# Kernel tuning notes

Measured on AMD Instinct MI355X. Metric: run time of the kernel, lower is better.

## Reference

```python
import jax, jax.numpy as jnp
import numpy as np

OUT = 128
HEADS = 8
HEAD = OUT // HEADS
NEG_SLOPE = 0.01


def _seg_softmax(logits, seg, num_segments):
    # logits: [E, H]; seg: [E] receiver node ids
    mx = jax.ops.segment_max(logits, seg, num_segments=num_segments)
    e = jnp.exp(logits - mx[seg])
    s = jax.ops.segment_sum(e, seg, num_segments=num_segments)
    return e / s[seg]


def _gat_pass(z, src, tgt, extra_logits, Wm, bm, Wa1, ba1, Wa2, ba2):
    # z: [N, 2D]; src/tgt: [E]; extra_logits: [E, H] or None
    N = z.shape[0]
    att1 = z @ Wa1 + ba1  # [N, H]
    att2 = z @ Wa2 + ba2  # [N, H]
    logits = att1[src] + att2[tgt]
    if extra_logits is not None:
        logits = logits + extra_logits
    coefs = _seg_softmax(jax.nn.leaky_relu(logits, NEG_SLOPE), tgt, N)  # [E, H]
    v = (z @ Wm + bm).reshape(N, HEADS, HEAD)  # [N, H, hs]
    msg = coefs[..., None] * v[src]            # [E, H, hs]
    agg = jax.ops.segment_sum(msg, tgt, num_segments=N)  # [N, H, hs]
    return agg.reshape(N, OUT)


def setup_inputs() -> dict:
    key = jax.random.key(0)
    ks = jax.random.split(key, 16)
    B, N, D, E = 2, 32768, 128, 262144
    ZD = 2 * D  # concat(node_fts, hidden)
    inp = {
        "node_fts": jax.random.normal(ks[0], (B, N, D), jnp.float32),
        "gkt_edge_fts": jax.random.normal(ks[1], (B, E, D), jnp.float32),
        "hidden": jax.random.normal(ks[2], (B, N, D), jnp.float32),
        "cfg_indices_padded": jax.random.randint(ks[3], (B, E, 2), 0, N, jnp.int32),
        "gkt_indices_padded": jax.random.randint(ks[4], (B, E, 2), 0, N, jnp.int32),
        "Wm": jax.random.normal(ks[5], (ZD, OUT), jnp.float32) / np.sqrt(ZD),
        "bm": jnp.zeros((OUT,), jnp.float32),
        "Wskip": jax.random.normal(ks[6], (ZD, OUT), jnp.float32) / np.sqrt(ZD),
        "bskip": jnp.zeros((OUT,), jnp.float32),
        "Wa1": jax.random.normal(ks[7], (ZD, HEADS), jnp.float32) / np.sqrt(ZD),
        "ba1": jnp.zeros((HEADS,), jnp.float32),
        "Wa2": jax.random.normal(ks[8], (ZD, HEADS), jnp.float32) / np.sqrt(ZD),
        "ba2": jnp.zeros((HEADS,), jnp.float32),
        "Wae": jax.random.normal(ks[9], (D, HEADS), jnp.float32) / np.sqrt(D),
        "bae": jnp.zeros((HEADS,), jnp.float32),
    }
    return inp


def reference(node_fts, gkt_edge_fts, hidden, cfg_indices_padded, gkt_indices_padded,
              Wm, bm, Wskip, bskip, Wa1, ba1, Wa2, ba2, Wae, bae):
    cfg_src = cfg_indices_padded[..., 0]
    cfg_tgt = cfg_indices_padded[..., 1]
    gkt_src = gkt_indices_padded[..., 0]
    gkt_tgt = gkt_indices_padded[..., 1]

    # ---- cfg stage ----
    cfg_z = jnp.concatenate([node_fts, hidden], axis=-1)  # [B, N, 2D]

    def cfg_one(z_b, src_b, tgt_b):
        return _gat_pass(z_b, src_b, tgt_b, None, Wm, bm, Wa1, ba1, Wa2, ba2)

    cfg_hidden = jax.vmap(cfg_one)(cfg_z, cfg_src, cfg_tgt)  # [B, N, OUT]
    cfg_hidden = cfg_hidden + cfg_z @ Wskip + bskip  # residual skip
    cfg_hidden = jax.nn.relu(cfg_hidden)

    # ---- gkt stage ----
    gkt_z = jnp.concatenate([node_fts, cfg_hidden], axis=-1)  # [B, N, 2D]
    gkt_att_e = gkt_edge_fts @ Wae + bae  # [B, E, H]

    def gkt_one(z_b, src_b, tgt_b, ae_b):
        return _gat_pass(z_b, src_b, tgt_b, ae_b, Wm, bm, Wa1, ba1, Wa2, ba2)

    ret = jax.vmap(gkt_one)(gkt_z, gkt_src, gkt_tgt, gkt_att_e)  # [B, N, OUT]
    ret = ret + gkt_z @ Wskip + bskip
    ret = jax.nn.relu(ret)
    return ret
```

## Files before the change

kernel.cpp:

```cpp
#include <hip/hip_runtime.h>
#include <hip/hip_bf16.h>

#define NB 2
#define NN 32768
#define NE 262144
#define DD 128
#define ZD 256
#define HEADS 8
#define OUTD 128
#define CAP 64

typedef short s16x8 __attribute__((ext_vector_type(8)));
typedef float f32x4 __attribute__((ext_vector_type(4)));
#define MFMA(a,b,c) __builtin_amdgcn_mfma_f32_16x16x32_bf16((a),(b),(c),0,0,0)

__device__ inline ushort f2bf(float f) {
    union { float f; unsigned u; } c; c.f = f;
    unsigned u = c.u;
    unsigned r = (u + 0x7fffu + ((u >> 16) & 1u)) >> 16;
    return (ushort)r;
}
__device__ inline float bf2f(ushort u) {
    union { unsigned u; float f; } c; c.u = ((unsigned)u) << 16;
    return c.f;
}

__global__ __launch_bounds__(256) void pack_w(
    const float* __restrict__ Wm, const float* __restrict__ Wsk,
    const float* __restrict__ Wa1, const float* __restrict__ Wa2,
    const float* __restrict__ bm, const float* __restrict__ bsk,
    const float* __restrict__ ba1, const float* __restrict__ ba2,
    ushort* __restrict__ WT, float* __restrict__ bias)
{
    int c = blockIdx.x;
    int k = threadIdx.x;
    float val;
    if (c < 32) {
        int a = c & 15;
        float w = (a < 8) ? Wa1[k*8 + a] : Wa2[k*8 + (a - 8)];
        if (c < 16) val = w;
        else { ushort hi = f2bf(w); val = w - bf2f(hi); }
    } else if (c < 160) {
        val = Wm[k*128 + (c - 32)];
    } else {
        val = Wsk[k*128 + (c - 160)];
    }
    WT[((size_t)(k >> 5)*288 + c)*32 + (k & 31)] = f2bf(val);
    if (k == 0) {
        if (c < 16) bias[c] = (c < 8) ? ba1[c] : ba2[c - 8];
        else if (c >= 32) bias[c - 16] = (c < 160) ? bm[c - 32] : bsk[c - 160];
    }
}

__global__ __launch_bounds__(256) void bucket_kernel(
    const int* __restrict__ cfg, const int* __restrict__ gkt,
    int* __restrict__ cnt, int2* __restrict__ pairs)
{
    int gid = blockIdx.x*256 + threadIdx.x;
    int L = gid >> 18, e = gid & (NE - 1);
    const int* base = (L < 2) ? cfg : gkt;
    const int* ip = base + (((size_t)(L & 1) << 18) + e)*2;
    int src = ip[0], tgt = ip[1];
    int pos = atomicAdd(&cnt[(L << 15) + tgt], 1);
    if (pos < CAP)
        pairs[((size_t)((L << 15) + tgt) << 6) + pos] = make_int2(e, src);
}

__global__ __launch_bounds__(256) void edge_att(
    const float* __restrict__ efts, const float* __restrict__ Wae,
    const float* __restrict__ bae, float* __restrict__ out)
{
    int t = threadIdx.x, lane = t & 63, wid = t >> 6;
    int col = lane & 15, q = lane >> 4;
    s16x8 bf[4];
    #pragma unroll
    for (int kc = 0; kc < 4; ++kc) {
        #pragma unroll
        for (int j = 0; j < 8; ++j) {
            float wv = (col < 8) ? Wae[(kc*32 + q*8 + j)*8 + col] : 0.f;
            bf[kc][j] = (short)f2bf(wv);
        }
    }
    float bb = (col < 8) ? bae[col] : 0.f;
    int wg = blockIdx.x*4 + wid;
    const int NT = (NB*NE)/16;
    for (int tile = wg; tile < NT; tile += gridDim.x*4) {
        size_t row = (size_t)tile*16 + col;
        const float* rp = efts + row*128 + q*8;
        f32x4 acc = {0.f, 0.f, 0.f, 0.f};
        #pragma unroll
        for (int kc = 0; kc < 4; ++kc) {
            float4 x0 = *(const float4*)(rp + kc*32);
            float4 x1 = *(const float4*)(rp + kc*32 + 4);
            s16x8 af;
            af[0] = (short)f2bf(x0.x); af[1] = (short)f2bf(x0.y);
            af[2] = (short)f2bf(x0.z); af[3] = (short)f2bf(x0.w);
            af[4] = (short)f2bf(x1.x); af[5] = (short)f2bf(x1.y);
            af[6] = (short)f2bf(x1.z); af[7] = (short)f2bf(x1.w);
            acc = MFMA(af, bf[kc], acc);
        }
        if (col < 8) {
            size_t e0 = (size_t)tile*16 + q*4;
            #pragma unroll
            for (int r = 0; r < 4; ++r)
                out[(e0 + r)*8 + col] = acc[r] + bb;
        }
    }
}

__global__ __launch_bounds__(256) void gemm_nodes(
    const float* __restrict__ nf, const float* __restrict__ h2,
    const ushort* __restrict__ WT, const float* __restrict__ bias,
    float* __restrict__ att1, float* __restrict__ att2,
    float* __restrict__ vout, float* __restrict__ skip)
{
    constexpr int LDA = 264;
    __shared__ ushort Ah[32*LDA];
    __shared__ ushort Al[32*LDA];
    int t = threadIdx.x;
    int row0 = blockIdx.x * 32;

    #pragma unroll
    for (int it = 0; it < 8; ++it) {
        int flat = it*256 + t;
        int r = flat >> 6, c4 = flat & 63;
        size_t gr = (size_t)row0 + r;
        const float* sp = (c4 < 32) ? (nf + gr*128 + c4*4)
                                    : (h2 + gr*128 + (c4 - 32)*4);
        float4 x = *(const float4*)sp;
        ushort4 hi, lo;
        hi.x = f2bf(x.x); lo.x = f2bf(x.x - bf2f(hi.x));
        hi.y = f2bf(x.y); lo.y = f2bf(x.y - bf2f(hi.y));
        hi.z = f2bf(x.z); lo.z = f2bf(x.z - bf2f(hi.z));
        hi.w = f2bf(x.w); lo.w = f2bf(x.w - bf2f(hi.w));
        *(ushort4*)&Ah[r*LDA + c4*4] = hi;
        *(ushort4*)&Al[r*LDA + c4*4] = lo;
    }
    __syncthreads();

    int lane = t & 63, wid = t >> 6;
    int rg = wid >> 1, nh = wid & 1;
    int q = lane >> 4, c = lane & 15;
    int mr = rg*16 + c;
    f32x4 zero = {0.f, 0.f, 0.f, 0.f};
    f32x4 acc[9];
    #pragma unroll
    for (int i = 0; i < 9; ++i) acc[i] = zero;

    const ushort* Wb = WT + (size_t)c*32 + q*8;
    #pragma unroll
    for (int ks = 0; ks < 8; ++ks) {
        const ushort* Wk = Wb + (size_t)ks*288*32;
        s16x8 ah = *(const s16x8*)&Ah[mr*LDA + ks*32 + q*8];
        if (nh == 0) {
            s16x8 al = *(const s16x8*)&Al[mr*LDA + ks*32 + q*8];
            s16x8 bh = *(const s16x8*)&Wk[0];
            s16x8 bl = *(const s16x8*)&Wk[16*32];
            acc[0] = MFMA(ah, bh, acc[0]);
            acc[0] = MFMA(al, bh, acc[0]);
            acc[0] = MFMA(ah, bl, acc[0]);
            #pragma unroll
            for (int j = 1; j < 8; ++j) {
                s16x8 bb = *(const s16x8*)&Wk[(16 + 16*j)*32];
                acc[j] = MFMA(ah, bb, acc[j]);
            }
        } else {
            #pragma unroll
            for (int j = 0; j < 9; ++j) {
                s16x8 bb = *(const s16x8*)&Wk[(144 + 16*j)*32];
                acc[j] = MFMA(ah, bb, acc[j]);
            }
        }
    }

    int rowb = row0 + rg*16 + q*4;
    if (nh == 0) {
        float bsv = bias[c];
        #pragma unroll
        for (int r = 0; r < 4; ++r) {
            size_t row = (size_t)rowb + r;
            float val = acc[0][r] + bsv;
            if (c < 8) att1[row*8 + c] = val;
            else       att2[row*8 + (c - 8)] = val;
        }
        #pragma unroll
        for (int j = 1; j < 8; ++j) {
            int col = (j - 1)*16 + c;
            float bv = bias[16 + col];
            #pragma unroll
            for (int r = 0; r < 4; ++r) {
                size_t row = (size_t)rowb + r;
                vout[row*128 + col] = acc[j][r] + bv;
            }
        }
    } else {
        {
            int col = 112 + c;
            float bv = bias[16 + col];
            #pragma unroll
            for (int r = 0; r < 4; ++r) {
                size_t row = (size_t)rowb + r;
                vout[row*128 + col] = acc[0][r] + bv;
            }
        }
        #pragma unroll
        for (int j = 1; j < 9; ++j) {
            int col = (j - 1)*16 + c;
            float bv = bias[144 + col];
            #pragma unroll
            for (int r = 0; r < 4; ++r) {
                size_t row = (size_t)rowb + r;
                skip[row*128 + col] = acc[j][r] + bv;
            }
        }
    }
}

__global__ __launch_bounds__(256) void agg_kernel(
    const int* __restrict__ cnt, const int2* __restrict__ pairs,
    const float* __restrict__ att1, const float* __restrict__ att2,
    const float* __restrict__ v, const float* __restrict__ skip,
    const float* __restrict__ ae, float* __restrict__ out, int listBase)
{
    int t = threadIdx.x;
    int wid = t >> 6, lane = t & 63;
    int g = blockIdx.x*4 + wid;
    int b = g >> 15, n = g & (NN - 1);
    int L = listBase + b;
    int slot = lane >> 5, c4 = lane & 31, h = c4 >> 2;
    int deg = cnt[(L << 15) + n];
    if (deg > CAP) deg = CAP;
    const int2* pr = pairs + ((size_t)((L << 15) + n) << 6);
    int bN = b << 15;
    size_t bE8 = ((size_t)b << 18)*8;
    float a2 = att2[(size_t)g*8 + h];
    float4 acc = {0.f, 0.f, 0.f, 0.f};
    float den = 0.f;
    for (int base = 0; base < deg; base += 8) {
        int ei[4], pe[4], ps[4];
        #pragma unroll
        for (int j = 0; j < 4; ++j) {
            int e = base + j*2 + slot;
            ei[j] = e;
            int idx = (e < deg) ? e : 0;
            int2 pp = pr[idx];
            pe[j] = pp.x; ps[j] = pp.y;
        }
        #pragma unroll
        for (int j = 0; j < 4; ++j) {
            float4 vv = *(const float4*)&v[(size_t)(bN + ps[j])*128 + c4*4];
            float a1 = att1[(size_t)(bN + ps[j])*8 + h];
            float l = a1 + a2;
            if (ae) l += ae[bE8 + (size_t)pe[j]*8 + h];
            l = (l < 0.f) ? 0.01f*l : l;
            float w = (ei[j] < deg) ? __expf(l) : 0.f;
            den += w;
            acc.x = fmaf(w, vv.x, acc.x);
            acc.y = fmaf(w, vv.y, acc.y);
            acc.z = fmaf(w, vv.z, acc.z);
            acc.w = fmaf(w, vv.w, acc.w);
        }
    }
    den   += __shfl_xor(den, 32);
    acc.x += __shfl_xor(acc.x, 32);
    acc.y += __shfl_xor(acc.y, 32);
    acc.z += __shfl_xor(acc.z, 32);
    acc.w += __shfl_xor(acc.w, 32);
    if (slot == 0) {
        float inv = (deg > 0) ? 1.f/den : 0.f;
        float4 sk = *(const float4*)&skip[(size_t)g*128 + c4*4];
        float4 o;
        o.x = fmaxf(fmaf(acc.x, inv, sk.x), 0.f);
        o.y = fmaxf(fmaf(acc.y, inv, sk.y), 0.f);
        o.z = fmaxf(fmaf(acc.z, inv, sk.z), 0.f);
        o.w = fmaxf(fmaf(acc.w, inv, sk.w), 0.f);
        *(float4*)&out[(size_t)g*128 + c4*4] = o;
    }
}

extern "C" void kernel_launch(void* const* d_in, const int* in_sizes, int n_in,
                              void* d_out, int out_size, void* d_ws, size_t ws_size,
                              hipStream_t stream)
{
    const float* nf   = (const float*)d_in[0];
    const float* efts = (const float*)d_in[1];
    const float* hid  = (const float*)d_in[2];
    const int*   cfg  = (const int*)d_in[3];
    const int*   gkt  = (const int*)d_in[4];
    const float* Wm   = (const float*)d_in[5];
    const float* bm   = (const float*)d_in[6];
    const float* Wsk  = (const float*)d_in[7];
    const float* bsk  = (const float*)d_in[8];
    const float* Wa1  = (const float*)d_in[9];
    const float* ba1  = (const float*)d_in[10];
    const float* Wa2  = (const float*)d_in[11];
    const float* ba2  = (const float*)d_in[12];
    const float* Wae  = (const float*)d_in[13];
    const float* bae  = (const float*)d_in[14];

    char* p = (char*)d_ws;
    auto carve = [&](size_t bytes) -> char* {
        char* r = p; p += (bytes + 255) & ~(size_t)255; return r;
    };
    float*  att1 = (float*)carve((size_t)NB*NN*8*4);
    float*  att2 = (float*)carve((size_t)NB*NN*8*4);
    float*  vbuf = (float*)carve((size_t)NB*NN*128*4);
    float*  skip = (float*)carve((size_t)NB*NN*128*4);
    float*  cfgh = (float*)carve((size_t)NB*NN*128*4);
    float*  gae  = (float*)carve((size_t)NB*NE*8*4);
    ushort* WT   = (ushort*)carve((size_t)8*288*32*2);
    float*  bias = (float*)carve(288*4);
    int*    cnt  = (int*)carve((size_t)4*NN*4);
    int2*   pairs= (int2*)carve((size_t)4*NN*CAP*8);

    hipMemsetAsync(cnt, 0, (size_t)4*NN*4, stream);
    pack_w<<<288, 256, 0, stream>>>(Wm, Wsk, Wa1, Wa2, bm, bsk, ba1, ba2, WT, bias);
    bucket_kernel<<<(4*NE)/256, 256, 0, stream>>>(cfg, gkt, cnt, pairs);
    edge_att<<<1024, 256, 0, stream>>>(efts, Wae, bae, gae);

    gemm_nodes<<<(NB*NN)/32, 256, 0, stream>>>(nf, hid, WT, bias, att1, att2, vbuf, skip);
    agg_kernel<<<(NB*NN)/4, 256, 0, stream>>>(cnt, pairs, att1, att2, vbuf, skip, nullptr, cfgh, 0);

    gemm_nodes<<<(NB*NN)/32, 256, 0, stream>>>(nf, cfgh, WT, bias, att1, att2, vbuf, skip);
    agg_kernel<<<(NB*NN)/4, 256, 0, stream>>>(cnt, pairs, att1, att2, vbuf, skip, gae, (float*)d_out, 2);
}
```

Before: 738.6 us.

## Merge prep kernels into one launch, widen agg unroll, prefetch skip

Combines weight packing, edge bucketing and the edge-attention GEMM into one heterogeneous kernel that dispatches on block index. This removes two launches and lets the independent prep work run concurrently on the GPU. The edge-attention path now uses twice as many blocks and loads all inputs before converting them. The aggregation loop handles 16 edges per iteration instead of 8 to keep more gathers in flight, and the skip load is issued before the shuffle reduction. The cost is higher register pressure in agg_kernel and wasted lanes for low-degree nodes.

```diff
diff --git a/kernel.cpp b/kernel.cpp
--- a/kernel.cpp
+++ b/kernel.cpp
@@ -10,6 +10,10 @@
 #define OUTD 128
 #define CAP 64
 
+#define EA_BLOCKS 2048
+#define BK_BLOCKS 4096
+#define PK_BLOCKS 288
+
 typedef short s16x8 __attribute__((ext_vector_type(8)));
 typedef float f32x4 __attribute__((ext_vector_type(4)));
 #define MFMA(a,b,c) __builtin_amdgcn_mfma_f32_16x16x32_bf16((a),(b),(c),0,0,0)
@@ -25,85 +29,87 @@
     return c.f;
 }
 
-__global__ __launch_bounds__(256) void pack_w(
+__global__ __launch_bounds__(256) void prep_kernel(
+    const float* __restrict__ efts, const float* __restrict__ Wae,
+    const float* __restrict__ bae, float* __restrict__ gae,
+    const int* __restrict__ cfg, const int* __restrict__ gkt,
+    int* __restrict__ cnt, int2* __restrict__ pairs,
     const float* __restrict__ Wm, const float* __restrict__ Wsk,
     const float* __restrict__ Wa1, const float* __restrict__ Wa2,
     const float* __restrict__ bm, const float* __restrict__ bsk,
     const float* __restrict__ ba1, const float* __restrict__ ba2,
     ushort* __restrict__ WT, float* __restrict__ bias)
 {
-    int c = blockIdx.x;
-    int k = threadIdx.x;
-    float val;
-    if (c < 32) {
-        int a = c & 15;
-        float w = (a < 8) ? Wa1[k*8 + a] : Wa2[k*8 + (a - 8)];
-        if (c < 16) val = w;
-        else { ushort hi = f2bf(w); val = w - bf2f(hi); }
-    } else if (c < 160) {
-        val = Wm[k*128 + (c - 32)];
+    int bi = blockIdx.x;
+    int t = threadIdx.x;
+
+    if (bi < EA_BLOCKS) {
+        int lane = t & 63, wid = t >> 6;
+        int col = lane & 15, q = lane >> 4;
+        s16x8 bf[4];
+        #pragma unroll
+        for (int kc = 0; kc < 4; ++kc) {
+            #pragma unroll
+            for (int j = 0; j < 8; ++j) {
+                float wv = (col < 8) ? Wae[(kc*32 + q*8 + j)*8 + col] : 0.f;
+                bf[kc][j] = (short)f2bf(wv);
+            }
+        }
+        float bb = (col < 8) ? bae[col] : 0.f;
+        int wg = bi*4 + wid;
+        const int NT = (NB*NE)/16;
+        for (int tile = wg; tile < NT; tile += EA_BLOCKS*4) {
+            const float* rp = efts + ((size_t)tile*16 + col)*128 + q*8;
+            float4 x0[4], x1[4];
+            #pragma unroll
+            for (int kc = 0; kc < 4; ++kc) {
+                x0[kc] = *(const float4*)(rp + kc*32);
+                x1[kc] = *(const float4*)(rp + kc*32 + 4);
+            }
+            f32x4 acc = {0.f, 0.f, 0.f, 0.f};
+            #pragma unroll
+            for (int kc = 0; kc < 4; ++kc) {
+                s16x8 af;
+                af[0] = (short)f2bf(x0[kc].x); af[1] = (short)f2bf(x0[kc].y);
+                af[2] = (short)f2bf(x0[kc].z); af[3] = (short)f2bf(x0[kc].w);
+                af[4] = (short)f2bf(x1[kc].x); af[5] = (short)f2bf(x1[kc].y);
+                af[6] = (short)f2bf(x1[kc].z); af[7] = (short)f2bf(x1[kc].w);
+                acc = MFMA(af, bf[kc], acc);
+            }
+            if (col < 8) {
+                size_t e0 = (size_t)tile*16 + q*4;
+                #pragma unroll
+                for (int r = 0; r < 4; ++r)
+                    gae[(e0 + r)*8 + col] = acc[r] + bb;
+            }
+        }
+    } else if (bi < EA_BLOCKS + BK_BLOCKS) {
+        int gid = (bi - EA_BLOCKS)*256 + t;
+        int L = gid >> 18, e = gid & (NE - 1);
+        const int* base = (L < 2) ? cfg : gkt;
+        const int* ip = base + (((size_t)(L & 1) << 18) + e)*2;
+        int src = ip[0], tgt = ip[1];
+        int pos = atomicAdd(&cnt[(L << 15) + tgt], 1);
+        if (pos < CAP)
+            pairs[((size_t)((L << 15) + tgt) << 6) + pos] = make_int2(e, src);
     } else {
-        val = Wsk[k*128 + (c - 160)];
-    }
-    WT[((size_t)(k >> 5)*288 + c)*32 + (k & 31)] = f2bf(val);
-    if (k == 0) {
-        if (c < 16) bias[c] = (c < 8) ? ba1[c] : ba2[c - 8];
-        else if (c >= 32) bias[c - 16] = (c < 160) ? bm[c - 32] : bsk[c - 160];
-    }
-}
-
-__global__ __launch_bounds__(256) void bucket_kernel(
-    const int* __restrict__ cfg, const int* __restrict__ gkt,
-    int* __restrict__ cnt, int2* __restrict__ pairs)
-{
-    int gid = blockIdx.x*256 + threadIdx.x;
-    int L = gid >> 18, e = gid & (NE - 1);
-    const int* base = (L < 2) ? cfg : gkt;
-    const int* ip = base + (((size_t)(L & 1) << 18) + e)*2;
-    int src = ip[0], tgt = ip[1];
-    int pos = atomicAdd(&cnt[(L << 15) + tgt], 1);
-    if (pos < CAP)
-        pairs[((size_t)((L << 15) + tgt) << 6) + pos] = make_int2(e, src);
-}
-
-__global__ __launch_bounds__(256) void edge_att(
-    const float* __restrict__ efts, const float* __restrict__ Wae,
-    const float* __restrict__ bae, float* __restrict__ out)
-{
-    int t = threadIdx.x, lane = t & 63, wid = t >> 6;
-    int col = lane & 15, q = lane >> 4;
-    s16x8 bf[4];
-    #pragma unroll
-    for (int kc = 0; kc < 4; ++kc) {
-        #pragma unroll
-        for (int j = 0; j < 8; ++j) {
-            float wv = (col < 8) ? Wae[(kc*32 + q*8 + j)*8 + col] : 0.f;
-            bf[kc][j] = (short)f2bf(wv);
-        }
-    }
-    float bb = (col < 8) ? bae[col] : 0.f;
-    int wg = blockIdx.x*4 + wid;
-    const int NT = (NB*NE)/16;
-    for (int tile = wg; tile < NT; tile += gridDim.x*4) {
-        size_t row = (size_t)tile*16 + col;
-        const float* rp = efts + row*128 + q*8;
-        f32x4 acc = {0.f, 0.f, 0.f, 0.f};
-        #pragma unroll
-        for (int kc = 0; kc < 4; ++kc) {
-            float4 x0 = *(const float4*)(rp + kc*32);
-            float4 x1 = *(const float4*)(rp + kc*32 + 4);
-            s16x8 af;
-            af[0] = (short)f2bf(x0.x); af[1] = (short)f2bf(x0.y);
-            af[2] = (short)f2bf(x0.z); af[3] = (short)f2bf(x0.w);
-            af[4] = (short)f2bf(x1.x); af[5] = (short)f2bf(x1.y);
-            af[6] = (short)f2bf(x1.z); af[7] = (short)f2bf(x1.w);
-            acc = MFMA(af, bf[kc], acc);
-        }
-        if (col < 8) {
-            size_t e0 = (size_t)tile*16 + q*4;
-            #pragma unroll
-            for (int r = 0; r < 4; ++r)
-                out[(e0 + r)*8 + col] = acc[r] + bb;
+        int c = bi - (EA_BLOCKS + BK_BLOCKS);
+        int k = t;
+        float val;
+        if (c < 32) {
+            int a = c & 15;
+            float w = (a < 8) ? Wa1[k*8 + a] : Wa2[k*8 + (a - 8)];
+            if (c < 16) val = w;
+            else { ushort hi = f2bf(w); val = w - bf2f(hi); }
+        } else if (c < 160) {
+            val = Wm[k*128 + (c - 32)];
+        } else {
+            val = Wsk[k*128 + (c - 160)];
+        }
+        WT[((size_t)(k >> 5)*288 + c)*32 + (k & 31)] = f2bf(val);
+        if (k == 0) {
+            if (c < 16) bias[c] = (c < 8) ? ba1[c] : ba2[c - 8];
+            else if (c >= 32) bias[c - 16] = (c < 160) ? bm[c - 32] : bsk[c - 160];
         }
     }
 }
@@ -236,10 +242,10 @@
     float a2 = att2[(size_t)g*8 + h];
     float4 acc = {0.f, 0.f, 0.f, 0.f};
     float den = 0.f;
-    for (int base = 0; base < deg; base += 8) {
-        int ei[4], pe[4], ps[4];
-        #pragma unroll
-        for (int j = 0; j < 4; ++j) {
+    for (int base = 0; base < deg; base += 16) {
+        int ei[8], pe[8], ps[8];
+        #pragma unroll
+        for (int j = 0; j < 8; ++j) {
             int e = base + j*2 + slot;
             ei[j] = e;
             int idx = (e < deg) ? e : 0;
@@ -247,7 +253,7 @@
             pe[j] = pp.x; ps[j] = pp.y;
         }
         #pragma unroll
-        for (int j = 0; j < 4; ++j) {
+        for (int j = 0; j < 8; ++j) {
             float4 vv = *(const float4*)&v[(size_t)(bN + ps[j])*128 + c4*4];
             float a1 = att1[(size_t)(bN + ps[j])*8 + h];
             float l = a1 + a2;
@@ -261,6 +267,7 @@
             acc.w = fmaf(w, vv.w, acc.w);
         }
     }
+    float4 sk = *(const float4*)&skip[(size_t)g*128 + c4*4];
     den   += __shfl_xor(den, 32);
     acc.x += __shfl_xor(acc.x, 32);
     acc.y += __shfl_xor(acc.y, 32);
@@ -268,7 +275,6 @@
     acc.w += __shfl_xor(acc.w, 32);
     if (slot == 0) {
         float inv = (deg > 0) ? 1.f/den : 0.f;
-        float4 sk = *(const float4*)&skip[(size_t)g*128 + c4*4];
         float4 o;
         o.x = fmaxf(fmaf(acc.x, inv, sk.x), 0.f);
         o.y = fmaxf(fmaf(acc.y, inv, sk.y), 0.f);
@@ -314,9 +320,9 @@
     int2*   pairs= (int2*)carve((size_t)4*NN*CAP*8);
 
     hipMemsetAsync(cnt, 0, (size_t)4*NN*4, stream);
-    pack_w<<<288, 256, 0, stream>>>(Wm, Wsk, Wa1, Wa2, bm, bsk, ba1, ba2, WT, bias);
-    bucket_kernel<<<(4*NE)/256, 256, 0, stream>>>(cfg, gkt, cnt, pairs);
-    edge_att<<<1024, 256, 0, stream>>>(efts, Wae, bae, gae);
+    prep_kernel<<<EA_BLOCKS + BK_BLOCKS + PK_BLOCKS, 256, 0, stream>>>(
+        efts, Wae, bae, gae, cfg, gkt, cnt, pairs,
+        Wm, Wsk, Wa1, Wa2, bm, bsk, ba1, ba2, WT, bias);
 
     gemm_nodes<<<(NB*NN)/32, 256, 0, stream>>>(nf, hid, WT, bias, att1, att2, vbuf, skip);
     agg_kernel<<<(NB*NN)/4, 256, 0, stream>>>(cnt, pairs, att1, att2, vbuf, skip, nullptr, cfgh, 0);
```

New measurement: 722.1 us. 2.2% less time.
